# Kernel optimization log

Hardware: AMD Instinct MI355X
Metric: run time of the kernel (lower is better)

Reference implementation:

```python
import jax, jax.numpy as jnp
import numpy as np
import math

B, H, S, D = 2, 16, 4096, 64

def setup_inputs() -> dict:
    key = jax.random.key(0)
    kq, kk, kv = jax.random.split(key, 3)
    q = jax.random.normal(kq, (B, H, S, D), dtype=jnp.float32)
    k = jax.random.normal(kk, (B, H, S, D), dtype=jnp.float32)
    v = jax.random.normal(kv, (B, H, S, D), dtype=jnp.float32)
    # causal mask: True above the diagonal means 'masked out' (matches masked_fill_)
    mask = ~jnp.tril(jnp.ones((S, S), dtype=bool))
    return {"q": q, "k": k, "v": v, "mask": mask}

def reference(q, k, v, mask):
    head_dim = q.shape[-1]
    scale = 1.0 / math.sqrt(head_dim)
    # scores: [B, H, S, S] -- same math as the chunked torch loop (chunking is a no-op mathematically)
    scores = jnp.einsum('bhqd,bhkd->bhqk', q, k) * scale
    scores = jnp.where(mask[None, None, :, :], -jnp.inf, scores)
    attn = jax.nn.softmax(scores, axis=-1)
    return jnp.einsum('bhqk,bhkd->bhqd', attn, v)
```

## Files before the change

### kernel.cpp

```cpp
#include <hip/hip_runtime.h>
#include <hip/hip_bf16.h>
#include <math.h>

#define SLEN 4096
#define DH   64
#define KVB  64
#define NHEAD 32
#define QBLK 128
#define NQT   (SLEN / QBLK)
#define TILE_E (KVB * DH)

typedef float  f32x4 __attribute__((ext_vector_type(4)));
typedef short  bf16x8 __attribute__((ext_vector_type(8)));
typedef unsigned short u16x8 __attribute__((ext_vector_type(8)));
typedef unsigned short u16x4 __attribute__((ext_vector_type(4)));
union U8 { u16x8 u; bf16x8 b; };
union U4 { unsigned d[4]; bf16x8 b; };

__device__ inline unsigned short f2bf(float f) {
    return __builtin_bit_cast(unsigned short, __float2bfloat16(f));
}
__device__ inline unsigned pk2(float lo, float hi_) {
    return (unsigned)f2bf(lo) | ((unsigned)f2bf(hi_) << 16);
}

__device__ inline void gload16(const unsigned short* g, unsigned short* l) {
    __builtin_amdgcn_global_load_lds(
        (const __attribute__((address_space(1))) void*)g,
        (__attribute__((address_space(3))) void*)l, 16, 0, 0);
}

extern "C" __global__ __launch_bounds__(512)
void prep_kv(const float* __restrict__ K, const float* __restrict__ V,
             unsigned short* __restrict__ Kb, unsigned short* __restrict__ Vt)
{
    const int tile = blockIdx.x & 63;
    const int head = blockIdx.x >> 6;
    const size_t gbase = (size_t)head * SLEN * DH + (size_t)tile * KVB * DH;
    const size_t tbase = ((size_t)head * 64 + tile) * TILE_E;
    const int tid = threadIdx.x;
    if (blockIdx.y == 0) {
        const int row = tid >> 3, d0 = (tid & 7) * 8;
        const float* src = K + gbase + (size_t)row * DH + d0;
        f32x4 a = *(const f32x4*)src, b = *(const f32x4*)(src + 4);
        u16x8 o;
        #pragma unroll
        for (int j = 0; j < 4; ++j) { o[j] = f2bf(a[j]); o[4 + j] = f2bf(b[j]); }
        *(u16x8*)&Kb[tbase + row * 64 + ((unsigned)d0 ^ ((row & 7) << 3))] = o;
    } else {
        const int kk = tid & 63, d0 = (tid >> 6) * 8;
        const int pos = ((kk >> 5) << 5) | (((kk & 15) >> 2) << 3)
                      | (((kk >> 4) & 1) << 2) | (kk & 3);
        const float* src = V + gbase + (size_t)kk * DH + d0;
        f32x4 a = *(const f32x4*)src, b = *(const f32x4*)(src + 4);
        #pragma unroll
        for (int j = 0; j < 8; ++j) {
            const int d = d0 + j;
            const float x = (j < 4) ? a[j] : b[j - 4];
            Vt[tbase + d * 64 + ((unsigned)pos ^ ((d & 7) << 3))] = f2bf(x);
        }
    }
}

extern "C" __global__ __launch_bounds__(256, 4)
void fa_fwd_v12(const float* __restrict__ Q, float* __restrict__ O,
                const unsigned short* __restrict__ Kb,
                const unsigned short* __restrict__ Vt)
{
    const int tid  = threadIdx.x;
    const int lane = tid & 63;
    const int w    = tid >> 6;
    const int l15  = lane & 15;
    const int l4   = lane >> 4;

    const int bid  = (int)blockIdx.x;
    const int qt   = (NQT - 1) - (bid >> 5);
    const int head = bid & 31;
    const size_t qbase  = (size_t)head * SLEN * DH;
    const size_t kvbase = (size_t)head * 64 * TILE_E;

    __shared__ __align__(16) unsigned short Kl[2][TILE_E];
    __shared__ __align__(16) unsigned short Vl[2][TILE_E];

    const float QSC = 0.125f * 1.44269504088896340736f;

    U8 ones;
    #pragma unroll
    for (int j = 0; j < 8; ++j) ones.u[j] = 0x3F80;

    const unsigned short* ksrc = Kb + kvbase;
    const unsigned short* vsrc = Vt + kvbase;

    const int q0   = qt * QBLK;
    const int ntl  = 2 * qt + 2;
    const int wq0  = q0 + w * 32;
    const int qg0  = wq0 + l15;
    const int qg1  = wq0 + 16 + l15;

    auto stage = [&](int b, int t) {
        const size_t toff = (size_t)t * TILE_E;
        const int ib = w * 2;
        gload16(ksrc + toff + ib * 512 + lane * 8,       &Kl[b][ib * 512]);
        gload16(ksrc + toff + (ib + 1) * 512 + lane * 8, &Kl[b][(ib + 1) * 512]);
        gload16(vsrc + toff + ib * 512 + lane * 8,       &Vl[b][ib * 512]);
        gload16(vsrc + toff + (ib + 1) * 512 + lane * 8, &Vl[b][(ib + 1) * 512]);
    };

    stage(0, 0);

    bf16x8 aq0[2], aq1[2];
    {
        const float* qp0 = Q + qbase + (size_t)qg0 * DH + l4 * 8;
        const float* qp1 = Q + qbase + (size_t)qg1 * DH + l4 * 8;
        #pragma unroll
        for (int ch = 0; ch < 2; ++ch) {
            f32x4 f0 = *(const f32x4*)(qp0 + ch * 32);
            f32x4 f1 = *(const f32x4*)(qp0 + ch * 32 + 4);
            U4 u;
            u.d[0] = pk2(f0[0] * QSC, f0[1] * QSC);
            u.d[1] = pk2(f0[2] * QSC, f0[3] * QSC);
            u.d[2] = pk2(f1[0] * QSC, f1[1] * QSC);
            u.d[3] = pk2(f1[2] * QSC, f1[3] * QSC);
            aq0[ch] = u.b;
            f0 = *(const f32x4*)(qp1 + ch * 32);
            f1 = *(const f32x4*)(qp1 + ch * 32 + 4);
            u.d[0] = pk2(f0[0] * QSC, f0[1] * QSC);
            u.d[1] = pk2(f0[2] * QSC, f0[3] * QSC);
            u.d[2] = pk2(f1[0] * QSC, f1[1] * QSC);
            u.d[3] = pk2(f1[2] * QSC, f1[3] * QSC);
            aq1[ch] = u.b;
        }
    }

    f32x4 acc0[4] = {}, acc1[4] = {};
    f32x4 lrow0 = {}, lrow1 = {};

    asm volatile("s_waitcnt vmcnt(0)" ::: "memory");
    __builtin_amdgcn_s_barrier();

    int cb = 0;
    for (int t = 0; t < ntl; ++t) {
        const int k0 = t * KVB;
        if (t + 1 < ntl) stage(cb ^ 1, t + 1);

        const bool live1 = (k0 <= wq0 + 31);
        if (live1) {
            const bool live0 = (k0 <= wq0 + 15);
            const unsigned short* Kc = &Kl[cb][0];
            const unsigned short* Vc = &Vl[cb][0];

            __builtin_amdgcn_s_setprio(1);
            f32x4 s0[4], s1[4];
            #pragma unroll
            for (int nt = 0; nt < 4; ++nt) {
                const int row = nt * 16 + l15;
                const unsigned rb = (unsigned)row * 64, sw = (unsigned)((row & 7) << 3);
                U8 ak0, ak1;
                ak0.u = *(const u16x8*)&Kc[rb + ((unsigned)(l4 * 8) ^ sw)];
                ak1.u = *(const u16x8*)&Kc[rb + ((unsigned)(32 + l4 * 8) ^ sw)];
                if (live0) {
                    f32x4 z = {};
                    z = __builtin_amdgcn_mfma_f32_16x16x32_bf16(ak0.b, aq0[0], z, 0, 0, 0);
                    s0[nt] = __builtin_amdgcn_mfma_f32_16x16x32_bf16(ak1.b, aq0[1], z, 0, 0, 0);
                }
                f32x4 z1 = {};
                z1 = __builtin_amdgcn_mfma_f32_16x16x32_bf16(ak0.b, aq1[0], z1, 0, 0, 0);
                s1[nt] = __builtin_amdgcn_mfma_f32_16x16x32_bf16(ak1.b, aq1[1], z1, 0, 0, 0);
            }
            __builtin_amdgcn_s_setprio(0);

            if (live0 && (k0 + KVB - 1 > wq0)) {
                #pragma unroll
                for (int nt = 0; nt < 4; ++nt)
                    #pragma unroll
                    for (int r = 0; r < 4; ++r)
                        if (k0 + nt * 16 + l4 * 4 + r > qg0) s0[nt][r] = -INFINITY;
            }
            if (k0 + KVB - 1 > wq0 + 16) {
                #pragma unroll
                for (int nt = 0; nt < 4; ++nt)
                    #pragma unroll
                    for (int r = 0; r < 4; ++r)
                        if (k0 + nt * 16 + l4 * 4 + r > qg1) s1[nt][r] = -INFINITY;
            }

            U4 u00, u01, u10, u11;
            if (live0) {
                u00.d[0] = pk2(exp2f(s0[0][0]), exp2f(s0[0][1]));
                u00.d[1] = pk2(exp2f(s0[0][2]), exp2f(s0[0][3]));
                u00.d[2] = pk2(exp2f(s0[1][0]), exp2f(s0[1][1]));
                u00.d[3] = pk2(exp2f(s0[1][2]), exp2f(s0[1][3]));
                u01.d[0] = pk2(exp2f(s0[2][0]), exp2f(s0[2][1]));
                u01.d[1] = pk2(exp2f(s0[2][2]), exp2f(s0[2][3]));
                u01.d[2] = pk2(exp2f(s0[3][0]), exp2f(s0[3][1]));
                u01.d[3] = pk2(exp2f(s0[3][2]), exp2f(s0[3][3]));
            }
            u10.d[0] = pk2(exp2f(s1[0][0]), exp2f(s1[0][1]));
            u10.d[1] = pk2(exp2f(s1[0][2]), exp2f(s1[0][3]));
            u10.d[2] = pk2(exp2f(s1[1][0]), exp2f(s1[1][1]));
            u10.d[3] = pk2(exp2f(s1[1][2]), exp2f(s1[1][3]));
            u11.d[0] = pk2(exp2f(s1[2][0]), exp2f(s1[2][1]));
            u11.d[1] = pk2(exp2f(s1[2][2]), exp2f(s1[2][3]));
            u11.d[2] = pk2(exp2f(s1[3][0]), exp2f(s1[3][1]));
            u11.d[3] = pk2(exp2f(s1[3][2]), exp2f(s1[3][3]));

            __builtin_amdgcn_s_setprio(1);
            if (live0) {
                lrow0 = __builtin_amdgcn_mfma_f32_16x16x32_bf16(u00.b, ones.b, lrow0, 0, 0, 0);
                lrow0 = __builtin_amdgcn_mfma_f32_16x16x32_bf16(u01.b, ones.b, lrow0, 0, 0, 0);
            }
            lrow1 = __builtin_amdgcn_mfma_f32_16x16x32_bf16(u10.b, ones.b, lrow1, 0, 0, 0);
            lrow1 = __builtin_amdgcn_mfma_f32_16x16x32_bf16(u11.b, ones.b, lrow1, 0, 0, 0);
            #pragma unroll
            for (int nt = 0; nt < 4; ++nt) {
                const int row = nt * 16 + l15;
                const unsigned rb = (unsigned)row * 64, sw = (unsigned)((row & 7) << 3);
                U8 vb0, vb1;
                vb0.u = *(const u16x8*)&Vc[rb + ((unsigned)(l4 * 8) ^ sw)];
                vb1.u = *(const u16x8*)&Vc[rb + ((unsigned)(32 + l4 * 8) ^ sw)];
                if (live0) {
                    acc0[nt] = __builtin_amdgcn_mfma_f32_16x16x32_bf16(u00.b, vb0.b, acc0[nt], 0, 0, 0);
                    acc0[nt] = __builtin_amdgcn_mfma_f32_16x16x32_bf16(u01.b, vb1.b, acc0[nt], 0, 0, 0);
                }
                acc1[nt] = __builtin_amdgcn_mfma_f32_16x16x32_bf16(u10.b, vb0.b, acc1[nt], 0, 0, 0);
                acc1[nt] = __builtin_amdgcn_mfma_f32_16x16x32_bf16(u11.b, vb1.b, acc1[nt], 0, 0, 0);
            }
            __builtin_amdgcn_s_setprio(0);
        }

        asm volatile("s_waitcnt vmcnt(0)" ::: "memory");
        __builtin_amdgcn_s_barrier();
        cb ^= 1;
    }

    #pragma unroll
    for (int r = 0; r < 4; ++r) {
        const float inv0 = 1.f / lrow0[r];
        const float inv1 = 1.f / lrow1[r];
        float* op0 = O + qbase + (size_t)(wq0 + l4 * 4 + r) * DH + l15;
        float* op1 = O + qbase + (size_t)(wq0 + 16 + l4 * 4 + r) * DH + l15;
        #pragma unroll
        for (int nt = 0; nt < 4; ++nt) {
            op0[nt * 16] = acc0[nt][r] * inv0;
            op1[nt * 16] = acc1[nt][r] * inv1;
        }
    }
}

#define QBLK4 128
#define KPAD 72
#define NQT4  (SLEN/QBLK4)
#define NPAIR4 (NQT4/2)

extern "C" __global__ __launch_bounds__(256)
void fa_fwd_causal(const float* __restrict__ Q, const float* __restrict__ K,
                   const float* __restrict__ V, float* __restrict__ O)
{
    const int tid  = threadIdx.x;
    const int lane = tid & 63;
    const int w    = tid >> 6;
    const int l15  = lane & 15;
    const int l4   = lane >> 4;

    const int bid  = (int)blockIdx.x;
    const int work = (bid & 7) * (NPAIR4 * NHEAD / 8) + (bid >> 3);
    const int head = work >> 4;
    const int pr   = work & (NPAIR4 - 1);
    const size_t base = (size_t)head * SLEN * DH;

    __shared__ unsigned short Kl[2][KVB * KPAD];
    __shared__ unsigned short Vt[2][DH * KPAD];
    __shared__ unsigned short Plds[4][16 * KPAD];

    const float QSC = 0.125f * 1.44269504088896340736f;
    const int krow = tid >> 2,        kc0 = (tid & 3) * 16;
    const int vd0  = (tid >> 4) * 4,  vk0 = (tid & 15) * 4;

    #pragma unroll 1
    for (int ph = 0; ph < 2; ++ph) {
        const int qt  = ph ? (NQT4 - 1 - pr) : pr;
        const int q0  = qt * QBLK4;
        const int ntl = 2 * qt + 2;
        const int qwave = q0 + w * 32;

        bf16x8 aq[2][2];
        #pragma unroll
        for (int set = 0; set < 2; ++set) {
            const int qr = q0 + w * 32 + set * 16 + l15;
            const float* qp = Q + base + (size_t)qr * DH + l4 * 8;
            #pragma unroll
            for (int ch = 0; ch < 2; ++ch) {
                f32x4 f0 = *(const f32x4*)(qp + ch * 32);
                f32x4 f1 = *(const f32x4*)(qp + ch * 32 + 4);
                U8 u;
                #pragma unroll
                for (int j = 0; j < 4; ++j) { u.u[j] = f2bf(f0[j] * QSC); u.u[4 + j] = f2bf(f1[j] * QSC); }
                aq[set][ch] = u.b;
            }
        }

        f32x4 acc[2][4] = {};
        float mrun[2] = { -INFINITY, -INFINITY };
        float lrun[2] = { 0.f, 0.f };
        f32x4 kreg[4], vreg[4];

        auto g_load = [&](int t) {
            const float* kp = K + base + (size_t)(t * KVB + krow) * DH + kc0;
            #pragma unroll
            for (int i = 0; i < 4; ++i) kreg[i] = *(const f32x4*)(kp + i * 4);
            const float* vp = V + base + (size_t)(t * KVB + vk0) * DH + vd0;
            #pragma unroll
            for (int i = 0; i < 4; ++i) vreg[i] = *(const f32x4*)(vp + (size_t)i * DH);
        };
        auto s_write = [&](int c) {
            unsigned short tmp[16];
            #pragma unroll
            for (int i = 0; i < 4; ++i)
                #pragma unroll
                for (int j = 0; j < 4; ++j) tmp[i * 4 + j] = f2bf(kreg[i][j]);
            unsigned short* kd = &Kl[c][krow * KPAD + kc0];
            *(u16x8*)kd       = *(u16x8*)&tmp[0];
            *(u16x8*)(kd + 8) = *(u16x8*)&tmp[8];
            #pragma unroll
            for (int i = 0; i < 4; ++i) {
                u16x4 pk;
                pk[0] = f2bf(vreg[0][i]); pk[1] = f2bf(vreg[1][i]);
                pk[2] = f2bf(vreg[2][i]); pk[3] = f2bf(vreg[3][i]);
                *(u16x4*)&Vt[c][(vd0 + i) * KPAD + vk0] = pk;
            }
        };

        g_load(0); s_write(0); g_load(1);
        __syncthreads();

        for (int t = 0; t < ntl; ++t) {
            const int c  = t & 1;
            const int k0 = t * KVB;
            if (t + 1 < ntl) { s_write(c ^ 1); if (t + 2 < ntl) g_load(t + 2); }

            if (k0 <= qwave + 31) {
                #pragma unroll
                for (int set = 0; set < 2; ++set) {
                    const int qs0 = qwave + set * 16;
                    if (k0 > qs0 + 15) continue;
                    const int q = qs0 + l15;

                    f32x4 s[4];
                    #pragma unroll
                    for (int nt = 0; nt < 4; ++nt) {
                        U8 ak0, ak1;
                        ak0.u = *(const u16x8*)&Kl[c][(nt*16 + l15) * KPAD + l4*8];
                        ak1.u = *(const u16x8*)&Kl[c][(nt*16 + l15) * KPAD + 32 + l4*8];
                        f32x4 z = {};
                        z = __builtin_amdgcn_mfma_f32_16x16x32_bf16(ak0.b, aq[set][0], z, 0, 0, 0);
                        z = __builtin_amdgcn_mfma_f32_16x16x32_bf16(ak1.b, aq[set][1], z, 0, 0, 0);
                        s[nt] = z;
                    }
                    if (k0 + KVB - 1 > qs0) {
                        #pragma unroll
                        for (int nt = 0; nt < 4; ++nt)
                            #pragma unroll
                            for (int r = 0; r < 4; ++r)
                                if (k0 + nt*16 + l4*4 + r > q) s[nt][r] = -INFINITY;
                    }
                    float mx = s[0][0];
                    #pragma unroll
                    for (int nt = 0; nt < 4; ++nt)
                        #pragma unroll
                        for (int r = 0; r < 4; ++r)
                            if (!(nt == 0 && r == 0)) mx = fmaxf(mx, s[nt][r]);
                    mx = fmaxf(mx, __shfl_xor(mx, 16));
                    mx = fmaxf(mx, __shfl_xor(mx, 32));
                    float mn = fmaxf(mrun[set], mx);
                    float fr = exp2f(mrun[set] - mn);
                    mrun[set] = mn;
                    float p[4][4];
                    float rs = 0.f;
                    #pragma unroll
                    for (int nt = 0; nt < 4; ++nt)
                        #pragma unroll
                        for (int r = 0; r < 4; ++r) {
                            float e = exp2f(s[nt][r] - mn);
                            p[nt][r] = e; rs += e;
                        }
                    rs += __shfl_xor(rs, 16);
                    rs += __shfl_xor(rs, 32);
                    lrun[set] = lrun[set] * fr + rs;

                    unsigned short* Pw = &Plds[w][0];
                    #pragma unroll
                    for (int nt = 0; nt < 4; ++nt) {
                        u16x4 pk;
                        pk[0] = f2bf(p[nt][0]); pk[1] = f2bf(p[nt][1]);
                        pk[2] = f2bf(p[nt][2]); pk[3] = f2bf(p[nt][3]);
                        *(u16x4*)&Pw[l15 * KPAD + nt*16 + l4*4] = pk;
                    }
                    #pragma unroll
                    for (int r = 0; r < 4; ++r) {
                        float frr = __shfl(fr, l4*4 + r);
                        #pragma unroll
                        for (int nt = 0; nt < 4; ++nt) acc[set][nt][r] *= frr;
                    }
                    asm volatile("s_waitcnt lgkmcnt(0)" ::: "memory");
                    __builtin_amdgcn_sched_barrier(0);
                    U8 pa0, pa1;
                    pa0.u = *(const u16x8*)&Pw[l15 * KPAD + l4*8];
                    pa1.u = *(const u16x8*)&Pw[l15 * KPAD + 32 + l4*8];
                    #pragma unroll
                    for (int nt = 0; nt < 4; ++nt) {
                        U8 vb0, vb1;
                        vb0.u = *(const u16x8*)&Vt[c][(nt*16 + l15) * KPAD + l4*8];
                        vb1.u = *(const u16x8*)&Vt[c][(nt*16 + l15) * KPAD + 32 + l4*8];
                        acc[set][nt] = __builtin_amdgcn_mfma_f32_16x16x32_bf16(pa0.b, vb0.b, acc[set][nt], 0, 0, 0);
                        acc[set][nt] = __builtin_amdgcn_mfma_f32_16x16x32_bf16(pa1.b, vb1.b, acc[set][nt], 0, 0, 0);
                    }
                }
            }
            __syncthreads();
        }
        #pragma unroll
        for (int set = 0; set < 2; ++set) {
            float inv = 1.f / lrun[set];
            #pragma unroll
            for (int r = 0; r < 4; ++r) {
                float invr = __shfl(inv, l4*4 + r);
                const int qrow = q0 + w*32 + set*16 + l4*4 + r;
                float* op = O + base + (size_t)qrow * DH + l15;
                #pragma unroll
                for (int nt = 0; nt < 4; ++nt)
                    op[nt*16] = acc[set][nt][r] * invr;
            }
        }
        __syncthreads();
    }
}

extern "C" void kernel_launch(void* const* d_in, const int* in_sizes, int n_in,
                              void* d_out, int out_size, void* d_ws, size_t ws_size,
                              hipStream_t stream) {
    (void)in_sizes; (void)n_in; (void)out_size;
    const float* q = (const float*)d_in[0];
    const float* k = (const float*)d_in[1];
    const float* v = (const float*)d_in[2];
    float* o = (float*)d_out;

    const size_t kv_elems = (size_t)NHEAD * 64 * TILE_E;
    const size_t need = 2 * kv_elems * sizeof(unsigned short);
    if (ws_size >= need) {
        unsigned short* Kb = (unsigned short*)d_ws;
        unsigned short* Vtw = Kb + kv_elems;
        prep_kv<<<dim3(NHEAD * 64, 2), 512, 0, stream>>>(k, v, Kb, Vtw);
        fa_fwd_v12<<<dim3(NQT * NHEAD), 256, 0, stream>>>(q, o, Kb, Vtw);
    } else {
        fa_fwd_causal<<<dim3(NPAIR4 * NHEAD), 256, 0, stream>>>(q, k, v, o);
    }
}
```

Measured before the change: 140.3 us.

## Triple-buffer K tiles with two-tile prefetch and reorder query-tile dispatch

K tiles now use a three-slot LDS ring and are prefetched two iterations ahead, while V keeps a double buffer prefetched one iteration ahead. The wait and barrier move to the top of the loop, with a partial vmcnt, so the newest K load can stay in flight during compute. This is meant to hide global-to-LDS latency behind the MFMA work. Query-tile dispatch order also changes from heaviest-first to an interleaved even/odd ordering. The extra 8KB of LDS per block may limit occupancy, and the new ordering may worsen tail balance.

```diff
diff --git a/kernel.cpp b/kernel.cpp
--- a/kernel.cpp
+++ b/kernel.cpp
@@ -63,7 +63,7 @@
 }
 
 extern "C" __global__ __launch_bounds__(256, 4)
-void fa_fwd_v12(const float* __restrict__ Q, float* __restrict__ O,
+void fa_fwd_v15(const float* __restrict__ Q, float* __restrict__ O,
                 const unsigned short* __restrict__ Kb,
                 const unsigned short* __restrict__ Vt)
 {
@@ -74,12 +74,13 @@
     const int l4   = lane >> 4;
 
     const int bid  = (int)blockIdx.x;
-    const int qt   = (NQT - 1) - (bid >> 5);
+    const int i32  = bid >> 5;
+    const int qt   = (i32 < 16) ? (2 * i32) : (63 - 2 * i32);
     const int head = bid & 31;
     const size_t qbase  = (size_t)head * SLEN * DH;
     const size_t kvbase = (size_t)head * 64 * TILE_E;
 
-    __shared__ __align__(16) unsigned short Kl[2][TILE_E];
+    __shared__ __align__(16) unsigned short Kl[3][TILE_E];
     __shared__ __align__(16) unsigned short Vl[2][TILE_E];
 
     const float QSC = 0.125f * 1.44269504088896340736f;
@@ -97,16 +98,22 @@
     const int qg0  = wq0 + l15;
     const int qg1  = wq0 + 16 + l15;
 
-    auto stage = [&](int b, int t) {
+    auto stageK = [&](int b, int t) {
         const size_t toff = (size_t)t * TILE_E;
         const int ib = w * 2;
         gload16(ksrc + toff + ib * 512 + lane * 8,       &Kl[b][ib * 512]);
         gload16(ksrc + toff + (ib + 1) * 512 + lane * 8, &Kl[b][(ib + 1) * 512]);
+    };
+    auto stageV = [&](int b, int t) {
+        const size_t toff = (size_t)t * TILE_E;
+        const int ib = w * 2;
         gload16(vsrc + toff + ib * 512 + lane * 8,       &Vl[b][ib * 512]);
         gload16(vsrc + toff + (ib + 1) * 512 + lane * 8, &Vl[b][(ib + 1) * 512]);
     };
 
-    stage(0, 0);
+    stageK(0, 0);
+    stageV(0, 0);
+    stageK(1, 1);
 
     bf16x8 aq0[2], aq1[2];
     {
@@ -135,19 +142,21 @@
     f32x4 acc0[4] = {}, acc1[4] = {};
     f32x4 lrow0 = {}, lrow1 = {};
 
-    asm volatile("s_waitcnt vmcnt(0)" ::: "memory");
-    __builtin_amdgcn_s_barrier();
-
-    int cb = 0;
+    int kb = 0, vb = 0;
     for (int t = 0; t < ntl; ++t) {
         const int k0 = t * KVB;
-        if (t + 1 < ntl) stage(cb ^ 1, t + 1);
+        if (t + 1 < ntl) asm volatile("s_waitcnt vmcnt(1)" ::: "memory");
+        else             asm volatile("s_waitcnt vmcnt(0)" ::: "memory");
+        __builtin_amdgcn_s_barrier();
+
+        if (t + 1 < ntl) stageV(vb ^ 1, t + 1);
+        if (t + 2 < ntl) stageK((kb == 0) ? 2 : kb - 1, t + 2);
 
         const bool live1 = (k0 <= wq0 + 31);
         if (live1) {
             const bool live0 = (k0 <= wq0 + 15);
-            const unsigned short* Kc = &Kl[cb][0];
-            const unsigned short* Vc = &Vl[cb][0];
+            const unsigned short* Kc = &Kl[kb][0];
+            const unsigned short* Vc = &Vl[vb][0];
 
             __builtin_amdgcn_s_setprio(1);
             f32x4 s0[4], s1[4];
@@ -228,9 +237,8 @@
             __builtin_amdgcn_s_setprio(0);
         }
 
-        asm volatile("s_waitcnt vmcnt(0)" ::: "memory");
-        __builtin_amdgcn_s_barrier();
-        cb ^= 1;
+        kb = (kb == 2) ? 0 : kb + 1;
+        vb ^= 1;
     }
 
     #pragma unroll
@@ -450,7 +458,7 @@
         unsigned short* Kb = (unsigned short*)d_ws;
         unsigned short* Vtw = Kb + kv_elems;
         prep_kv<<<dim3(NHEAD * 64, 2), 512, 0, stream>>>(k, v, Kb, Vtw);
-        fa_fwd_v12<<<dim3(NQT * NHEAD), 256, 0, stream>>>(q, o, Kb, Vtw);
+        fa_fwd_v15<<<dim3(NQT * NHEAD), 256, 0, stream>>>(q, o, Kb, Vtw);
     } else {
         fa_fwd_causal<<<dim3(NPAIR4 * NHEAD), 256, 0, stream>>>(q, k, v, o);
     }
```

After: 139.1 us. Within noise of the previous version (-0.9%).
